# Kernel optimization log

Measured on AMD Instinct MI355X. Metric: run time of the kernel, lower is better.

The kernel has to match this reference:

```python
import jax, jax.numpy as jnp
import numpy as np

B, C, H, W, K = 4, 64, 128, 128, 3
K2 = K * K
PAD = (K - 1) // 2  # same padding for 3x3


def setup_inputs() -> dict:
    key = jax.random.key(0)
    ks = jax.random.split(key, 9)
    s = 0.05
    return {
        "x": jax.random.normal(ks[0], (B, C, H, W), jnp.float32),
        "inter": jax.random.normal(ks[1], (B, C, H, W), jnp.float32),
        # offset/mask predictor conv: input cat([x, inter]) -> 3*K2 channels (dy, dx, mask)
        "w_offset": jax.random.normal(ks[2], (3 * K2, 2 * C, K, K), jnp.float32) * s,
        "b_offset": jnp.zeros((3 * K2,), jnp.float32),
        # deformable conv weight (bias=False per DGM init)
        "w_dcn": jax.random.normal(ks[3], (C, C, K, K), jnp.float32) * s,
        # SFT gamma branch: two 1x1 convs (bias=False)
        "w_g1": jax.random.normal(ks[4], (C, C), jnp.float32) * s,
        "w_g2": jax.random.normal(ks[5], (C, C), jnp.float32) * s,
        # SFT beta branch: two 1x1 convs (bias=False)
        "w_b1": jax.random.normal(ks[6], (C, C), jnp.float32) * s,
        "w_b2": jax.random.normal(ks[7], (C, C), jnp.float32) * s,
    }


def _lrelu(v):
    # LeakyReLU(0.1)
    return jnp.where(v >= 0, v, 0.1 * v)


def _conv(x, w, b=None):
    y = jax.lax.conv_general_dilated(
        x, w, window_strides=(1, 1), padding=[(PAD, PAD), (PAD, PAD)],
        dimension_numbers=("NCHW", "OIHW", "NCHW"))
    if b is not None:
        y = y + b[None, :, None, None]
    return y


def _bilinear_gather(x, py, px):
    """x: [B,C,H,W]; py, px: [B,K2,H,W] float sample coords.
    Returns samples [B,K2,H,W,C]; out-of-bounds treated as zero (DCN zero-pad)."""
    y0 = jnp.floor(py)
    x0 = jnp.floor(px)
    wy = (py - y0)[..., None]
    wx = (px - x0)[..., None]

    def gather(yi, xi):
        valid = ((yi >= 0) & (yi < H) & (xi >= 0) & (xi < W)).astype(x.dtype)
        yc = jnp.clip(yi, 0, H - 1).astype(jnp.int32)
        xc = jnp.clip(xi, 0, W - 1).astype(jnp.int32)
        bidx = jnp.arange(B)[:, None, None, None]
        v = x[bidx, :, yc, xc]  # advanced indexing -> [B,K2,H,W,C]
        return v * valid[..., None]

    v00 = gather(y0, x0)
    v01 = gather(y0, x0 + 1)
    v10 = gather(y0 + 1, x0)
    v11 = gather(y0 + 1, x0 + 1)
    return (v00 * (1 - wy) * (1 - wx) + v01 * (1 - wy) * wx
            + v10 * wy * (1 - wx) + v11 * wy * wx)


def _dgm_forward(x, inter, w_offset, b_offset, w_dcn, w_g1, w_g2, w_b1, w_b2):
    # --- WADCN branch: modulated deformable conv, offsets predicted from cat(x, inter)
    om = _conv(jnp.concatenate([x, inter], axis=1), w_offset, b_offset)  # [B,3K2,H,W]
    dy, dx, m = jnp.split(om, 3, axis=1)  # each [B,K2,H,W]
    mask = jax.nn.sigmoid(m)

    ky, kx = jnp.meshgrid(jnp.arange(K), jnp.arange(K), indexing="ij")
    ky = ky.reshape(K2).astype(x.dtype)
    kx = kx.reshape(K2).astype(x.dtype)
    hh = jnp.arange(H, dtype=x.dtype)
    ww = jnp.arange(W, dtype=x.dtype)
    # sample coords: base grid + kernel-tap offset + learned offset
    py = hh[None, None, :, None] + (ky - PAD)[None, :, None, None] + dy  # [B,K2,H,W]
    px = ww[None, None, None, :] + (kx - PAD)[None, :, None, None] + dx

    samp = _bilinear_gather(x, py, px) * mask[..., None]  # [B,K2,H,W,C]
    dcn_out = jnp.einsum("bkhwc,ock->bohw", samp, w_dcn.reshape(C, C, K2))

    # --- SFT branch: two 1x1-conv + LeakyReLU chains producing gamma/beta
    gamma = jnp.einsum("oc,bchw->bohw", w_g2,
                       _lrelu(jnp.einsum("oc,bchw->bohw", w_g1, inter)))
    beta = jnp.einsum("oc,bchw->bohw", w_b2,
                      _lrelu(jnp.einsum("oc,bchw->bohw", w_b1, inter)))
    sft_out = x * gamma + beta

    # --- fused residual combine (DGM.relu is defined but never applied)
    return x + dcn_out + sft_out


def reference(x, inter, w_offset, b_offset, w_dcn, w_g1, w_g2, w_b1, w_b2):
    return _dgm_forward(x, inter, w_offset, b_offset, w_dcn, w_g1, w_g2, w_b1, w_b2)
```

## Files before the change

### kernel.cpp

```cpp
#include <hip/hip_runtime.h>
#include <hip/hip_bf16.h>
#include <math.h>

#define BB 4
#define CC 64
#define HH 128
#define WW 128
#define HW (HH*WW)
#define NPIX (BB*HW)

typedef __attribute__((ext_vector_type(8))) short short8;
typedef __attribute__((ext_vector_type(4))) float f32x4;

__device__ __forceinline__ float bf2f(ushort u) {
  union { unsigned u; float f; } v; v.u = ((unsigned)u) << 16; return v.f;
}
__device__ __forceinline__ ushort f2bf(float f) {
  __hip_bfloat16 h = __float2bfloat16(f); return *(ushort*)&h;
}

__global__ __launch_bounds__(256) void k_transp(
    const float* __restrict__ x, const float* __restrict__ inter,
    ushort* __restrict__ x_clh, ushort* __restrict__ inter_clh) {
  __shared__ float tile[64 * 129];
  int blk = blockIdx.x;
  int sel = blk >> 9;
  int bh = blk & 511;
  int b = bh >> 7, h = bh & 127;
  const float* src = sel ? inter : x;
  ushort* dst = sel ? inter_clh : x_clh;
  const float* sp = src + (size_t)(b * 64) * HW + h * WW;
  for (int i = threadIdx.x; i < 64 * 128; i += 256) {
    int c = i >> 7, w = i & 127;
    tile[c * 129 + w] = sp[(size_t)c * HW + w];
  }
  __syncthreads();
  ushort* dp = dst + ((size_t)b * HW + h * WW) * 64;
  for (int i = threadIdx.x; i < 64 * 128; i += 256) {
    int w = i >> 6, c = i & 63;
    dp[w * 64 + c] = f2bf(tile[c * 129 + w]);
  }
}

__global__ void k_wprep(const float* __restrict__ w_off,
                        const float* __restrict__ w_dcn,
                        const float* __restrict__ wg1, const float* __restrict__ wb1,
                        const float* __restrict__ wg2, const float* __restrict__ wb2,
                        ushort* __restrict__ wfb, ushort* __restrict__ wdT,
                        ushort* __restrict__ w1gb, ushort* __restrict__ w1bb,
                        ushort* __restrict__ w2gb, ushort* __restrict__ w2bb,
                        float* __restrict__ zp) {
  int blk = blockIdx.x;
  if (blk < 144) {
    int i = blk * 256 + threadIdx.x;
    if (i < 64) zp[i] = 0.f;
    if (i < 9 * 32 * 128) {
      int tap = i >> 12, rem = i & 4095, m = rem >> 7, c = rem & 127;
      float v = (m < 27) ? w_off[(size_t)(m * 128 + c) * 9 + tap] : 0.f;
      wfb[i] = f2bf(v);
    }
  } else if (blk < 288) {
    int i = (blk - 144) * 256 + threadIdx.x;
    if (i < 64 * 64 * 9) {
      int o = i / 576, rem = i % 576, k = rem >> 6, c = rem & 63;
      wdT[i] = f2bf(w_dcn[(o * 64 + c) * 9 + k]);
    }
  } else {
    int i = (blk - 288) * 256 + threadIdx.x;
    int m = i >> 12, j = i & 4095;
    const float* src = (m == 0) ? wg1 : (m == 1) ? wb1 : (m == 2) ? wg2 : wb2;
    ushort* dst = (m == 0) ? w1gb : (m == 1) ? w1bb : (m == 2) ? w2gb : w2bb;
    dst[j] = f2bf(src[j]);
  }
}

#define FPITCH 72

__global__ __launch_bounds__(256) void k_sft(
    const float* __restrict__ x, const ushort* __restrict__ inter_clh,
    const ushort* __restrict__ w1gb, const ushort* __restrict__ w1bb,
    const ushort* __restrict__ w2gb, const ushort* __restrict__ w2bb,
    float* __restrict__ out) {
  __shared__ ushort Sg[64 * FPITCH];
  __shared__ ushort Sb[64 * FPITCH];
  int tid = threadIdx.x;
  int lane = tid & 63;
  int quad = lane >> 4, col = lane & 15;
  int pg0 = blockIdx.x * 64;
  int b = pg0 >> 14, hw0 = pg0 & 16383;
  int o_base = __builtin_amdgcn_readfirstlane((tid >> 6) * 16);

  f32x4 ag[4], ab[4];
#pragma unroll
  for (int nt = 0; nt < 4; ++nt) {
    ag[nt] = (f32x4){0.f, 0.f, 0.f, 0.f};
    ab[nt] = (f32x4){0.f, 0.f, 0.f, 0.f};
  }
#pragma unroll
  for (int ks = 0; ks < 2; ++ks) {
    short8 a_g = *(const short8*)(w1gb + (size_t)(o_base + col) * 64 + ks * 32 + quad * 8);
    short8 a_b = *(const short8*)(w1bb + (size_t)(o_base + col) * 64 + ks * 32 + quad * 8);
#pragma unroll
    for (int nt = 0; nt < 4; ++nt) {
      short8 bf = *(const short8*)(inter_clh + (size_t)(pg0 + nt * 16 + col) * 64 + ks * 32 + quad * 8);
      ag[nt] = __builtin_amdgcn_mfma_f32_16x16x32_bf16(a_g, bf, ag[nt], 0, 0, 0);
      ab[nt] = __builtin_amdgcn_mfma_f32_16x16x32_bf16(a_b, bf, ab[nt], 0, 0, 0);
    }
  }
#pragma unroll
  for (int nt = 0; nt < 4; ++nt) {
    int px = nt * 16 + col;
    ushort pkg[4], pkb[4];
#pragma unroll
    for (int r = 0; r < 4; ++r) {
      float vg = ag[nt][r]; vg = vg >= 0.f ? vg : 0.1f * vg;
      float vb = ab[nt][r]; vb = vb >= 0.f ? vb : 0.1f * vb;
      pkg[r] = f2bf(vg); pkb[r] = f2bf(vb);
    }
    *(uint2*)(&Sg[px * FPITCH + o_base + quad * 4]) = *(uint2*)pkg;
    *(uint2*)(&Sb[px * FPITCH + o_base + quad * 4]) = *(uint2*)pkb;
  }
  __syncthreads();

  f32x4 gg[4], gb[4];
#pragma unroll
  for (int nt = 0; nt < 4; ++nt) {
    gg[nt] = (f32x4){0.f, 0.f, 0.f, 0.f};
    gb[nt] = (f32x4){0.f, 0.f, 0.f, 0.f};
  }
#pragma unroll
  for (int ks = 0; ks < 2; ++ks) {
    short8 a_g = *(const short8*)(w2gb + (size_t)(o_base + col) * 64 + ks * 32 + quad * 8);
    short8 a_b = *(const short8*)(w2bb + (size_t)(o_base + col) * 64 + ks * 32 + quad * 8);
#pragma unroll
    for (int nt = 0; nt < 4; ++nt) {
      short8 bg = *(const short8*)(Sg + (nt * 16 + col) * FPITCH + ks * 32 + quad * 8);
      short8 bb = *(const short8*)(Sb + (nt * 16 + col) * FPITCH + ks * 32 + quad * 8);
      gg[nt] = __builtin_amdgcn_mfma_f32_16x16x32_bf16(a_g, bg, gg[nt], 0, 0, 0);
      gb[nt] = __builtin_amdgcn_mfma_f32_16x16x32_bf16(a_b, bb, gb[nt], 0, 0, 0);
    }
  }

#pragma unroll
  for (int nt = 0; nt < 4; ++nt) {
#pragma unroll
    for (int r = 0; r < 4; ++r) {
      int o = o_base + quad * 4 + r;
      size_t idx = (size_t)(b * 64 + o) * HW + hw0 + nt * 16 + col;
      float xv = x[idx];
      out[idx] = xv + xv * gg[nt][r] + gb[nt][r];
    }
  }
}

#define CPITCH 72

__global__ __launch_bounds__(256) void k_convm(
    const ushort* __restrict__ x_clh, const ushort* __restrict__ inter_clh,
    const ushort* __restrict__ wfb, float* __restrict__ om) {
  __shared__ ushort S[6 * 34 * CPITCH];
  int tid = threadIdx.x;
  int wave = tid >> 6, lane = tid & 63;
  int quad = lane >> 4, col = lane & 15;
  int blk = blockIdx.x;
  int b = blk >> 9, h = (blk >> 2) & 127, wq = blk & 3;
  int pt = wave >> 1, mt = wave & 1;

  {
    int ch = (tid & 7) * 8;
    unsigned bbase = (unsigned)b * HW;
#pragma unroll
    for (int it = 0; it < 7; ++it) {
      int e = it * 32 + (tid >> 3);
      if (e < 204) {
        int srcrow = e / 34, pxl = e % 34;
        int src = srcrow / 3, row = srcrow % 3;
        int hs = h + row - 1;
        int ps = wq * 32 + pxl - 1;
        bool ok = ((unsigned)hs < 128u) && ((unsigned)ps < 128u);
        int hc = hs < 0 ? 0 : (hs > 127 ? 127 : hs);
        int pc = ps < 0 ? 0 : (ps > 127 ? 127 : ps);
        const ushort* sb = src ? inter_clh : x_clh;
        short8 v = *(const short8*)(sb + ((size_t)(bbase + (hc << 7) + pc)) * 64 + ch);
        short8 z = {0, 0, 0, 0, 0, 0, 0, 0};
        if (!ok) v = z;
        *(short8*)(&S[e * CPITCH + ch]) = v;
      }
    }
  }
  __syncthreads();

  f32x4 accx = {0.f, 0.f, 0.f, 0.f}, acci = {0.f, 0.f, 0.f, 0.f};
  const ushort* wb0 = wfb + (size_t)(mt * 16 + col) * 128 + quad * 8;
  int pxb = pt * 16 + col;

#pragma unroll
  for (int ky = 0; ky < 3; ++ky) {
#pragma unroll
    for (int kx = 0; kx < 3; ++kx) {
      int tap = ky * 3 + kx;
      const ushort* wt = wb0 + (size_t)tap * 4096;
#pragma unroll
      for (int ks = 0; ks < 2; ++ks) {
        short8 a0 = *(const short8*)(wt + ks * 32);
        short8 b0 = *(const short8*)(&S[(ky * 34 + pxb + kx) * CPITCH + ks * 32 + quad * 8]);
        accx = __builtin_amdgcn_mfma_f32_16x16x32_bf16(a0, b0, accx, 0, 0, 0);
        short8 a1 = *(const short8*)(wt + 64 + ks * 32);
        short8 b1 = *(const short8*)(&S[((3 + ky) * 34 + pxb + kx) * CPITCH + ks * 32 + quad * 8]);
        acci = __builtin_amdgcn_mfma_f32_16x16x32_bf16(a1, b1, acci, 0, 0, 0);
      }
    }
  }

  int pg = b * HW + h * WW + wq * 32 + pt * 16 + col;
#pragma unroll
  for (int r = 0; r < 4; ++r) {
    int o = mt * 16 + quad * 4 + r;
    float v = accx[r] + acci[r];
    if (o < 27) om[(size_t)o * NPIX + pg] = v;
  }
}

#define SPITCH 200
#define NPX 32

__global__ __launch_bounds__(256) void k_dcn(
    const ushort* __restrict__ x_clh, const float* __restrict__ om,
    const float* __restrict__ b_off, const ushort* __restrict__ wdT,
    const ushort* __restrict__ zp16,
    float* __restrict__ out) {
  __shared__ ushort S[NPX * SPITCH];
  __shared__ int   cy[9 * NPX], cx[9 * NPX];
  __shared__ float cwy[9 * NPX], cwx[9 * NPX], cm[9 * NPX];

  int tid = threadIdx.x;
  int wave = tid >> 6, lane = tid & 63;
  int quad = lane >> 4, col = lane & 15;
  int rr = lane >> 3, g = lane & 7;
  int pg0 = blockIdx.x * NPX;
  int b = pg0 >> 14;
  int o_base = __builtin_amdgcn_readfirstlane(wave * 16);

  for (int i = tid; i < 9 * NPX; i += 256) {
    int k = i >> 5, p = i & 31;
    int pg = pg0 + p;
    int hw = pg & 16383;
    int h = hw >> 7, w = hw & 127;
    float dy = om[(size_t)k * NPIX + pg] + b_off[k];
    float dx = om[(size_t)(9 + k) * NPIX + pg] + b_off[9 + k];
    float mz = om[(size_t)(18 + k) * NPIX + pg] + b_off[18 + k];
    float py = (float)(h + (k / 3) - 1) + dy;
    float px = (float)(w + (k % 3) - 1) + dx;
    float y0f = floorf(py), x0f = floorf(px);
    cy[i] = (int)y0f;
    cx[i] = (int)x0f;
    cwy[i] = py - y0f;
    cwx[i] = px - x0f;
    cm[i] = 1.f / (1.f + __expf(-mz));
  }

  f32x4 acc[2];
  acc[0] = (f32x4){0.f, 0.f, 0.f, 0.f};
  acc[1] = (f32x4){0.f, 0.f, 0.f, 0.f};

  const ushort* bp = x_clh + (size_t)b * HW * 64;

  for (int chunk = 0; chunk < 3; ++chunk) {
    __syncthreads();
#pragma unroll
    for (int it = 0; it < 3; ++it) {
      int p = wave * 8 + rr;
      int idx = (chunk * 3 + it) * NPX + p;
      int y0 = cy[idx], x0 = cx[idx];
      float wy = cwy[idx], wx = cwx[idx], m = cm[idx];
      bool yok0 = (unsigned)y0 < 128u, yok1 = (unsigned)(y0 + 1) < 128u;
      bool xok0 = (unsigned)x0 < 128u, xok1 = (unsigned)(x0 + 1) < 128u;
      const ushort* r0 = bp + ((size_t)(int)((y0 << 7) + x0)) * 64 + g * 8;
      const ushort* r1 = r0 + (size_t)WW * 64;
      short8 s00 = *(const short8*)((yok0 && xok0) ? r0 : zp16);
      short8 s01 = *(const short8*)((yok0 && xok1) ? (r0 + 64) : zp16);
      short8 s10 = *(const short8*)((yok1 && xok0) ? r1 : zp16);
      short8 s11 = *(const short8*)((yok1 && xok1) ? (r1 + 64) : zp16);
      short8 outv;
#pragma unroll
      for (int j = 0; j < 8; ++j) {
        float v00 = bf2f((ushort)s00[j]), v01 = bf2f((ushort)s01[j]);
        float v10 = bf2f((ushort)s10[j]), v11 = bf2f((ushort)s11[j]);
        float top = v00 + (v01 - v00) * wx;
        float bot = v10 + (v11 - v10) * wx;
        float val = top + (bot - top) * wy;
        outv[j] = (short)f2bf(val * m);
      }
      *(short8*)(&S[p * SPITCH + it * 64 + g * 8]) = outv;
    }
    __syncthreads();
    const ushort* wrow = wdT + (size_t)(o_base + col) * 576 + chunk * 192 + quad * 8;
    const ushort* srow = S + quad * 8;
#pragma unroll
    for (int ks = 0; ks < 6; ++ks) {
      short8 a = *(const short8*)(wrow + ks * 32);
#pragma unroll
      for (int nt = 0; nt < 2; ++nt) {
        short8 bf = *(const short8*)(srow + (nt * 16 + col) * SPITCH + ks * 32);
        acc[nt] = __builtin_amdgcn_mfma_f32_16x16x32_bf16(a, bf, acc[nt], 0, 0, 0);
      }
    }
  }

  int hw0 = pg0 & 16383;
#pragma unroll
  for (int nt = 0; nt < 2; ++nt) {
#pragma unroll
    for (int r = 0; r < 4; ++r) {
      int o = o_base + quad * 4 + r;
      size_t idx = (size_t)(b * 64 + o) * HW + hw0 + nt * 16 + col;
      out[idx] += acc[nt][r];
    }
  }
}

extern "C" void kernel_launch(void* const* d_in, const int* in_sizes, int n_in,
                              void* d_out, int out_size, void* d_ws, size_t ws_size,
                              hipStream_t stream) {
  const float* x     = (const float*)d_in[0];
  const float* inter = (const float*)d_in[1];
  const float* w_off = (const float*)d_in[2];
  const float* b_off = (const float*)d_in[3];
  const float* w_dcn = (const float*)d_in[4];
  const float* wg1   = (const float*)d_in[5];
  const float* wg2   = (const float*)d_in[6];
  const float* wb1   = (const float*)d_in[7];
  const float* wb2   = (const float*)d_in[8];
  float* out = (float*)d_out;

  float* ws        = (float*)d_ws;
  ushort* x_clh    = (ushort*)ws;
  ushort* inter_clh= (ushort*)(ws + 2097152);
  float* om        = ws + 4194304;
  ushort* wfb      = (ushort*)(ws + 5963776);
  ushort* wdT      = (ushort*)(ws + 5982208);
  ushort* w1gb     = (ushort*)(ws + 6000640);
  ushort* w1bb     = (ushort*)(ws + 6002688);
  ushort* w2gb     = (ushort*)(ws + 6004736);
  ushort* w2bb     = (ushort*)(ws + 6006784);
  float* zp        = ws + 6008832;

  k_transp<<<1024, 256, 0, stream>>>(x, inter, x_clh, inter_clh);
  k_wprep<<<352, 256, 0, stream>>>(w_off, w_dcn, wg1, wb1, wg2, wb2,
                                   wfb, wdT, w1gb, w1bb, w2gb, w2bb, zp);

  k_sft<<<1024, 256, 0, stream>>>(x, inter_clh, w1gb, w1bb, w2gb, w2bb, out);

  k_convm<<<2048, 256, 0, stream>>>(x_clh, inter_clh, wfb, om);

  k_dcn<<<2048, 256, 0, stream>>>(x_clh, om, b_off, wdT, (const ushort*)zp, out);
}
```

Before: 181.1 us.

## Fuse SFT branch into DCN kernel and merge prep kernels

Merges the transpose and weight-prep kernels into one launch, and folds the SFT 1x1-conv gamma/beta computation into the deformable-conv kernel so the final output is written once as x + x*gamma + beta + dcn. This removes a full fp32 write-then-read of the output tensor and two kernel launches. The shared memory for the SFT staging is aliased with the offset-coordinate arrays, separated by a barrier. It adds register pressure and extra MFMA work to the DCN kernel, which may reduce occupancy.

Result: no change. 178.4 us (-1.5%).

```diff
diff --git a/kernel.cpp b/kernel.cpp
--- a/kernel.cpp
+++ b/kernel.cpp
@@ -19,137 +19,55 @@
   __hip_bfloat16 h = __float2bfloat16(f); return *(ushort*)&h;
 }
 
-__global__ __launch_bounds__(256) void k_transp(
+__global__ __launch_bounds__(256) void k_prep(
     const float* __restrict__ x, const float* __restrict__ inter,
-    ushort* __restrict__ x_clh, ushort* __restrict__ inter_clh) {
+    const float* __restrict__ w_off, const float* __restrict__ w_dcn,
+    const float* __restrict__ wg1, const float* __restrict__ wb1,
+    const float* __restrict__ wg2, const float* __restrict__ wb2,
+    ushort* __restrict__ x_clh, ushort* __restrict__ inter_clh,
+    ushort* __restrict__ wfb, ushort* __restrict__ wdT,
+    ushort* __restrict__ w1gb, ushort* __restrict__ w1bb,
+    ushort* __restrict__ w2gb, ushort* __restrict__ w2bb,
+    float* __restrict__ zp) {
   __shared__ float tile[64 * 129];
   int blk = blockIdx.x;
-  int sel = blk >> 9;
-  int bh = blk & 511;
-  int b = bh >> 7, h = bh & 127;
-  const float* src = sel ? inter : x;
-  ushort* dst = sel ? inter_clh : x_clh;
-  const float* sp = src + (size_t)(b * 64) * HW + h * WW;
-  for (int i = threadIdx.x; i < 64 * 128; i += 256) {
-    int c = i >> 7, w = i & 127;
-    tile[c * 129 + w] = sp[(size_t)c * HW + w];
-  }
-  __syncthreads();
-  ushort* dp = dst + ((size_t)b * HW + h * WW) * 64;
-  for (int i = threadIdx.x; i < 64 * 128; i += 256) {
-    int w = i >> 6, c = i & 63;
-    dp[w * 64 + c] = f2bf(tile[c * 129 + w]);
-  }
-}
-
-__global__ void k_wprep(const float* __restrict__ w_off,
-                        const float* __restrict__ w_dcn,
-                        const float* __restrict__ wg1, const float* __restrict__ wb1,
-                        const float* __restrict__ wg2, const float* __restrict__ wb2,
-                        ushort* __restrict__ wfb, ushort* __restrict__ wdT,
-                        ushort* __restrict__ w1gb, ushort* __restrict__ w1bb,
-                        ushort* __restrict__ w2gb, ushort* __restrict__ w2bb,
-                        float* __restrict__ zp) {
-  int blk = blockIdx.x;
-  if (blk < 144) {
-    int i = blk * 256 + threadIdx.x;
+  if (blk < 1024) {
+    int sel = blk >> 9;
+    int bh = blk & 511;
+    int b = bh >> 7, h = bh & 127;
+    const float* src = sel ? inter : x;
+    ushort* dst = sel ? inter_clh : x_clh;
+    const float* sp = src + (size_t)(b * 64) * HW + h * WW;
+    for (int i = threadIdx.x; i < 64 * 128; i += 256) {
+      int c = i >> 7, w = i & 127;
+      tile[c * 129 + w] = sp[(size_t)c * HW + w];
+    }
+    __syncthreads();
+    ushort* dp = dst + ((size_t)b * HW + h * WW) * 64;
+    for (int i = threadIdx.x; i < 64 * 128; i += 256) {
+      int w = i >> 6, c = i & 63;
+      dp[w * 64 + c] = f2bf(tile[c * 129 + w]);
+    }
+  } else if (blk < 1168) {
+    int i = (blk - 1024) * 256 + threadIdx.x;
     if (i < 64) zp[i] = 0.f;
     if (i < 9 * 32 * 128) {
       int tap = i >> 12, rem = i & 4095, m = rem >> 7, c = rem & 127;
       float v = (m < 27) ? w_off[(size_t)(m * 128 + c) * 9 + tap] : 0.f;
       wfb[i] = f2bf(v);
     }
-  } else if (blk < 288) {
-    int i = (blk - 144) * 256 + threadIdx.x;
+  } else if (blk < 1312) {
+    int i = (blk - 1168) * 256 + threadIdx.x;
     if (i < 64 * 64 * 9) {
       int o = i / 576, rem = i % 576, k = rem >> 6, c = rem & 63;
       wdT[i] = f2bf(w_dcn[(o * 64 + c) * 9 + k]);
     }
   } else {
-    int i = (blk - 288) * 256 + threadIdx.x;
+    int i = (blk - 1312) * 256 + threadIdx.x;
     int m = i >> 12, j = i & 4095;
     const float* src = (m == 0) ? wg1 : (m == 1) ? wb1 : (m == 2) ? wg2 : wb2;
     ushort* dst = (m == 0) ? w1gb : (m == 1) ? w1bb : (m == 2) ? w2gb : w2bb;
     dst[j] = f2bf(src[j]);
-  }
-}
-
-#define FPITCH 72
-
-__global__ __launch_bounds__(256) void k_sft(
-    const float* __restrict__ x, const ushort* __restrict__ inter_clh,
-    const ushort* __restrict__ w1gb, const ushort* __restrict__ w1bb,
-    const ushort* __restrict__ w2gb, const ushort* __restrict__ w2bb,
-    float* __restrict__ out) {
-  __shared__ ushort Sg[64 * FPITCH];
-  __shared__ ushort Sb[64 * FPITCH];
-  int tid = threadIdx.x;
-  int lane = tid & 63;
-  int quad = lane >> 4, col = lane & 15;
-  int pg0 = blockIdx.x * 64;
-  int b = pg0 >> 14, hw0 = pg0 & 16383;
-  int o_base = __builtin_amdgcn_readfirstlane((tid >> 6) * 16);
-
-  f32x4 ag[4], ab[4];
-#pragma unroll
-  for (int nt = 0; nt < 4; ++nt) {
-    ag[nt] = (f32x4){0.f, 0.f, 0.f, 0.f};
-    ab[nt] = (f32x4){0.f, 0.f, 0.f, 0.f};
-  }
-#pragma unroll
-  for (int ks = 0; ks < 2; ++ks) {
-    short8 a_g = *(const short8*)(w1gb + (size_t)(o_base + col) * 64 + ks * 32 + quad * 8);
-    short8 a_b = *(const short8*)(w1bb + (size_t)(o_base + col) * 64 + ks * 32 + quad * 8);
-#pragma unroll
-    for (int nt = 0; nt < 4; ++nt) {
-      short8 bf = *(const short8*)(inter_clh + (size_t)(pg0 + nt * 16 + col) * 64 + ks * 32 + quad * 8);
-      ag[nt] = __builtin_amdgcn_mfma_f32_16x16x32_bf16(a_g, bf, ag[nt], 0, 0, 0);
-      ab[nt] = __builtin_amdgcn_mfma_f32_16x16x32_bf16(a_b, bf, ab[nt], 0, 0, 0);
-    }
-  }
-#pragma unroll
-  for (int nt = 0; nt < 4; ++nt) {
-    int px = nt * 16 + col;
-    ushort pkg[4], pkb[4];
-#pragma unroll
-    for (int r = 0; r < 4; ++r) {
-      float vg = ag[nt][r]; vg = vg >= 0.f ? vg : 0.1f * vg;
-      float vb = ab[nt][r]; vb = vb >= 0.f ? vb : 0.1f * vb;
-      pkg[r] = f2bf(vg); pkb[r] = f2bf(vb);
-    }
-    *(uint2*)(&Sg[px * FPITCH + o_base + quad * 4]) = *(uint2*)pkg;
-    *(uint2*)(&Sb[px * FPITCH + o_base + quad * 4]) = *(uint2*)pkb;
-  }
-  __syncthreads();
-
-  f32x4 gg[4], gb[4];
-#pragma unroll
-  for (int nt = 0; nt < 4; ++nt) {
-    gg[nt] = (f32x4){0.f, 0.f, 0.f, 0.f};
-    gb[nt] = (f32x4){0.f, 0.f, 0.f, 0.f};
-  }
-#pragma unroll
-  for (int ks = 0; ks < 2; ++ks) {
-    short8 a_g = *(const short8*)(w2gb + (size_t)(o_base + col) * 64 + ks * 32 + quad * 8);
-    short8 a_b = *(const short8*)(w2bb + (size_t)(o_base + col) * 64 + ks * 32 + quad * 8);
-#pragma unroll
-    for (int nt = 0; nt < 4; ++nt) {
-      short8 bg = *(const short8*)(Sg + (nt * 16 + col) * FPITCH + ks * 32 + quad * 8);
-      short8 bb = *(const short8*)(Sb + (nt * 16 + col) * FPITCH + ks * 32 + quad * 8);
-      gg[nt] = __builtin_amdgcn_mfma_f32_16x16x32_bf16(a_g, bg, gg[nt], 0, 0, 0);
-      gb[nt] = __builtin_amdgcn_mfma_f32_16x16x32_bf16(a_b, bb, gb[nt], 0, 0, 0);
-    }
-  }
-
-#pragma unroll
-  for (int nt = 0; nt < 4; ++nt) {
-#pragma unroll
-    for (int r = 0; r < 4; ++r) {
-      int o = o_base + quad * 4 + r;
-      size_t idx = (size_t)(b * 64 + o) * HW + hw0 + nt * 16 + col;
-      float xv = x[idx];
-      out[idx] = xv + xv * gg[nt][r] + gb[nt][r];
-    }
   }
 }
 
@@ -223,23 +141,84 @@
 
 #define SPITCH 200
 #define NPX 32
-
-__global__ __launch_bounds__(256) void k_dcn(
-    const ushort* __restrict__ x_clh, const float* __restrict__ om,
+#define FP32 72
+
+__global__ __launch_bounds__(256) void k_mega(
+    const float* __restrict__ x, const ushort* __restrict__ x_clh,
+    const ushort* __restrict__ inter_clh, const float* __restrict__ om,
     const float* __restrict__ b_off, const ushort* __restrict__ wdT,
-    const ushort* __restrict__ zp16,
-    float* __restrict__ out) {
+    const ushort* __restrict__ w1gb, const ushort* __restrict__ w1bb,
+    const ushort* __restrict__ w2gb, const ushort* __restrict__ w2bb,
+    const ushort* __restrict__ zp16, float* __restrict__ out) {
   __shared__ ushort S[NPX * SPITCH];
-  __shared__ int   cy[9 * NPX], cx[9 * NPX];
-  __shared__ float cwy[9 * NPX], cwx[9 * NPX], cm[9 * NPX];
+  __shared__ __align__(16) char U[2 * NPX * FP32 * 2];
+  ushort* Sg = (ushort*)U;
+  ushort* Sb = Sg + NPX * FP32;
+  int*   cy  = (int*)U;
+  int*   cx  = cy + 288;
+  float* cwy = (float*)(cx + 288);
+  float* cwx = cwy + 288;
+  float* cm  = cwx + 288;
 
   int tid = threadIdx.x;
   int wave = tid >> 6, lane = tid & 63;
   int quad = lane >> 4, col = lane & 15;
   int rr = lane >> 3, g = lane & 7;
   int pg0 = blockIdx.x * NPX;
-  int b = pg0 >> 14;
+  int b = pg0 >> 14, hw0 = pg0 & 16383;
   int o_base = __builtin_amdgcn_readfirstlane(wave * 16);
+
+  f32x4 ag[2], ab[2];
+#pragma unroll
+  for (int nt = 0; nt < 2; ++nt) {
+    ag[nt] = (f32x4){0.f, 0.f, 0.f, 0.f};
+    ab[nt] = (f32x4){0.f, 0.f, 0.f, 0.f};
+  }
+#pragma unroll
+  for (int ks = 0; ks < 2; ++ks) {
+    short8 a_g = *(const short8*)(w1gb + (size_t)(o_base + col) * 64 + ks * 32 + quad * 8);
+    short8 a_b = *(const short8*)(w1bb + (size_t)(o_base + col) * 64 + ks * 32 + quad * 8);
+#pragma unroll
+    for (int nt = 0; nt < 2; ++nt) {
+      short8 bf = *(const short8*)(inter_clh + (size_t)(pg0 + nt * 16 + col) * 64 + ks * 32 + quad * 8);
+      ag[nt] = __builtin_amdgcn_mfma_f32_16x16x32_bf16(a_g, bf, ag[nt], 0, 0, 0);
+      ab[nt] = __builtin_amdgcn_mfma_f32_16x16x32_bf16(a_b, bf, ab[nt], 0, 0, 0);
+    }
+  }
+#pragma unroll
+  for (int nt = 0; nt < 2; ++nt) {
+    int px = nt * 16 + col;
+    ushort pkg[4], pkb[4];
+#pragma unroll
+    for (int r = 0; r < 4; ++r) {
+      float vg = ag[nt][r]; vg = vg >= 0.f ? vg : 0.1f * vg;
+      float vb = ab[nt][r]; vb = vb >= 0.f ? vb : 0.1f * vb;
+      pkg[r] = f2bf(vg); pkb[r] = f2bf(vb);
+    }
+    *(uint2*)(&Sg[px * FP32 + o_base + quad * 4]) = *(uint2*)pkg;
+    *(uint2*)(&Sb[px * FP32 + o_base + quad * 4]) = *(uint2*)pkb;
+  }
+  __syncthreads();
+
+  f32x4 gg[2], gb[2];
+#pragma unroll
+  for (int nt = 0; nt < 2; ++nt) {
+    gg[nt] = (f32x4){0.f, 0.f, 0.f, 0.f};
+    gb[nt] = (f32x4){0.f, 0.f, 0.f, 0.f};
+  }
+#pragma unroll
+  for (int ks = 0; ks < 2; ++ks) {
+    short8 a_g = *(const short8*)(w2gb + (size_t)(o_base + col) * 64 + ks * 32 + quad * 8);
+    short8 a_b = *(const short8*)(w2bb + (size_t)(o_base + col) * 64 + ks * 32 + quad * 8);
+#pragma unroll
+    for (int nt = 0; nt < 2; ++nt) {
+      short8 bgf = *(const short8*)(Sg + (nt * 16 + col) * FP32 + ks * 32 + quad * 8);
+      short8 bbf = *(const short8*)(Sb + (nt * 16 + col) * FP32 + ks * 32 + quad * 8);
+      gg[nt] = __builtin_amdgcn_mfma_f32_16x16x32_bf16(a_g, bgf, gg[nt], 0, 0, 0);
+      gb[nt] = __builtin_amdgcn_mfma_f32_16x16x32_bf16(a_b, bbf, gb[nt], 0, 0, 0);
+    }
+  }
+  __syncthreads();
 
   for (int i = tid; i < 9 * NPX; i += 256) {
     int k = i >> 5, p = i & 31;
@@ -307,14 +286,14 @@
     }
   }
 
-  int hw0 = pg0 & 16383;
 #pragma unroll
   for (int nt = 0; nt < 2; ++nt) {
 #pragma unroll
     for (int r = 0; r < 4; ++r) {
       int o = o_base + quad * 4 + r;
       size_t idx = (size_t)(b * 64 + o) * HW + hw0 + nt * 16 + col;
-      out[idx] += acc[nt][r];
+      float xv = x[idx];
+      out[idx] = xv + xv * gg[nt][r] + gb[nt][r] + acc[nt][r];
     }
   }
 }
@@ -345,13 +324,13 @@
   ushort* w2bb     = (ushort*)(ws + 6006784);
   float* zp        = ws + 6008832;
 
-  k_transp<<<1024, 256, 0, stream>>>(x, inter, x_clh, inter_clh);
-  k_wprep<<<352, 256, 0, stream>>>(w_off, w_dcn, wg1, wb1, wg2, wb2,
-                                   wfb, wdT, w1gb, w1bb, w2gb, w2bb, zp);
-
-  k_sft<<<1024, 256, 0, stream>>>(x, inter_clh, w1gb, w1bb, w2gb, w2bb, out);
+  k_prep<<<1376, 256, 0, stream>>>(x, inter, w_off, w_dcn, wg1, wb1, wg2, wb2,
+                                   x_clh, inter_clh, wfb, wdT,
+                                   w1gb, w1bb, w2gb, w2bb, zp);
 
   k_convm<<<2048, 256, 0, stream>>>(x_clh, inter_clh, wfb, om);
 
-  k_dcn<<<2048, 256, 0, stream>>>(x_clh, om, b_off, wdT, (const ushort*)zp, out);
-}
+  k_mega<<<2048, 256, 0, stream>>>(x, x_clh, inter_clh, om, b_off, wdT,
+                                   w1gb, w1bb, w2gb, w2bb,
+                                   (const ushort*)zp, out);
+}
```
